# Optimization experiments

Measured on AMD Instinct MI355X. Metric: run time of the kernel, lower is better.

The kernel has to match this reference:

```python
import jax, jax.numpy as jnp
import numpy as np

LN_EPS = 1e-3  # keras LayerNormalization default epsilon
LEAKY_SLOPE = 0.2  # tf 'leaky_relu' default alpha


def layer_norm(x, gamma, beta):
    mu = jnp.mean(x, axis=-1, keepdims=True)
    var = jnp.mean(jnp.square(x - mu), axis=-1, keepdims=True)
    return (x - mu) * jax.lax.rsqrt(var + LN_EPS) * gamma + beta


def attention_head(q_in, kv_in, Wk, Wv, Wq, causal):
    # q_in: [b, sq, d], kv_in: [b, sk, d]
    K = jnp.einsum('bsd,de->bse', kv_in, Wk)
    V = jnp.einsum('bsd,de->bse', kv_in, Wv)
    Q = jnp.einsum('bsd,de->bse', q_in, Wq)
    sk = K.shape[1]
    # NOTE: original scales by sqrt(window_size_keys), i.e. key seq length
    scores = jnp.einsum('bqe,bke->bqk', Q, K) / jnp.sqrt(jnp.float32(sk))
    if causal:
        sq = Q.shape[1]
        mask = jnp.triu(jnp.full((sq, sk), -jnp.inf, dtype=scores.dtype), k=1)
        scores = scores + mask
    probs = jax.nn.softmax(scores, axis=-1)
    return jnp.einsum('bqk,bke->bqe', probs, V)


def setup_inputs() -> dict:
    key = jax.random.key(0)
    ks = jax.random.split(key, 12)
    B, S, D, H = 4, 4096, 256, 400
    p = lambda k, shp: jax.random.normal(k, shp, dtype=jnp.float32) * 0.1
    return {
        'inputs': jax.random.normal(ks[0], (B, S, D), dtype=jnp.float32),
        'context_sequence': jax.random.normal(ks[1], (B, S, D), dtype=jnp.float32),
        'sa_Wk': p(ks[2], (D, D)),
        'sa_Wv': p(ks[3], (D, D)),
        'sa_Wq': p(ks[4], (D, D)),
        'ca_Wk': p(ks[5], (D, D)),
        'ca_Wv': p(ks[6], (D, D)),
        'ca_Wq': p(ks[7], (D, D)),
        'W1': p(ks[8], (D, H)),
        'b1': jnp.zeros((H,), dtype=jnp.float32),
        'W2': p(ks[9], (H, D)),
        'b2': jnp.zeros((D,), dtype=jnp.float32),
        'gamma': jnp.ones((D,), dtype=jnp.float32),
        'beta': jnp.zeros((D,), dtype=jnp.float32),
    }


def reference(inputs, context_sequence, sa_Wk, sa_Wv, sa_Wq, ca_Wk, ca_Wv, ca_Wq,
              W1, b1, W2, b2, gamma, beta):
    # 1) masked self-attention + residual + LN (shared LN params)
    in_attn = attention_head(inputs, inputs, sa_Wk, sa_Wv, sa_Wq, causal=True)
    x = layer_norm(in_attn + inputs, gamma, beta)
    # 2) unmasked cross-attention (queries = x, keys/values = context) + residual + LN
    ctx_attn = attention_head(x, context_sequence, ca_Wk, ca_Wv, ca_Wq, causal=False)
    y = layer_norm(ctx_attn + x, gamma, beta)
    # 3) FFN (Dense 400 leaky_relu -> Dense emb) + residual + LN
    h = jax.nn.leaky_relu(jnp.einsum('bsd,dh->bsh', y, W1) + b1, negative_slope=LEAKY_SLOPE)
    ff = jnp.einsum('bsh,hd->bsd', h, W2) + b2
    return layer_norm(ff + y, gamma, beta)
```

## Files before the change

kernel.cpp:

```cpp
#include <hip/hip_runtime.h>

typedef __bf16  bf16x4 __attribute__((ext_vector_type(4)));
typedef __bf16  bf16x8 __attribute__((ext_vector_type(8)));
typedef float   f32x4  __attribute__((ext_vector_type(4)));
typedef unsigned int u32;

constexpr int BM = 128, BN = 128, BK = 32;

__device__ __forceinline__ void async_cp16(const __bf16* g, __bf16* lds) {
    __builtin_amdgcn_global_load_lds(
        (const __attribute__((address_space(1))) u32*)g,
        (__attribute__((address_space(3))) u32*)lds, 16, 0, 0);
}

__device__ __forceinline__ int swz(int row, int q) {
    return row * BK + (((q + (row >> 1)) & 3) << 3);
}

template<int EPI>
__launch_bounds__(256)
__global__ void gemm_nt(const __bf16* __restrict__ Aall, const __bf16* __restrict__ Ball,
                        const float* __restrict__ bias,
                        void* __restrict__ C0, void* __restrict__ C1, void* __restrict__ C2,
                        int N, int K, long ldb, long sA, long sB, long sC,
                        int nTx, int klen, long pstrideB)
{
    const int bx = blockIdx.x;
    const int chunk = bx / nTx;
    const int n0 = (bx - chunk * nTx) * BN;
    const int m0 = blockIdx.y * BM;
    const int bz = blockIdx.z;
    const int kbase = chunk * klen;

    const __bf16* A  = Aall + (long)bz * sA;
    const __bf16* Bt = Ball + (long)bz * sB;

    __shared__ alignas(16) __bf16 As[BM * BK];
    __shared__ alignas(16) __bf16 Bs[BN * BK];

    const int tid = threadIdx.x;
    const int wave = tid >> 6, lane = tid & 63;
    const int wm = (wave >> 1) * 64, wn = (wave & 1) * 64;
    const int quad = lane >> 4, l16 = lane & 15;

    const int row0 = tid >> 2, sl0 = tid & 3;
    const int ks0 = (sl0 - (row0 >> 1)) & 3;
    const int row1 = row0 + 64;
    const int ks1 = (sl0 - (row1 >> 1)) & 3;
    const __bf16* gA0 = A  + (long)(m0 + row0) * K + kbase + ks0 * 8;
    const __bf16* gA1 = A  + (long)(m0 + row1) * K + kbase + ks1 * 8;
    const __bf16* gB0 = Bt + (long)(n0 + row0) * ldb + kbase + ks0 * 8;
    const __bf16* gB1 = Bt + (long)(n0 + row1) * ldb + kbase + ks1 * 8;
    __bf16* ldsA0 = As + wave * 512;
    __bf16* ldsA1 = As + 2048 + wave * 512;
    __bf16* ldsB0 = Bs + wave * 512;
    __bf16* ldsB1 = Bs + 2048 + wave * 512;

    f32x4 acc[4][4];
    #pragma unroll
    for (int i = 0; i < 4; i++)
        #pragma unroll
        for (int j = 0; j < 4; j++) { f32x4 z = {0.f, 0.f, 0.f, 0.f}; acc[i][j] = z; }

    for (int kk = 0; kk < klen; kk += BK) {
        __syncthreads();
        async_cp16(gA0, ldsA0);
        async_cp16(gA1, ldsA1);
        async_cp16(gB0, ldsB0);
        async_cp16(gB1, ldsB1);
        gA0 += BK; gA1 += BK; gB0 += BK; gB1 += BK;
        __syncthreads();

        bf16x8 af[4], bg[4];
        #pragma unroll
        for (int i = 0; i < 4; i++) {
            af[i] = *(const bf16x8*)(As + swz(wm + i * 16 + l16, quad));
            bg[i] = *(const bf16x8*)(Bs + swz(wn + i * 16 + l16, quad));
        }
        #pragma unroll
        for (int i = 0; i < 4; i++)
            #pragma unroll
            for (int j = 0; j < 4; j++)
                acc[i][j] = __builtin_amdgcn_mfma_f32_16x16x32_bf16(af[i], bg[j], acc[i][j], 0, 0, 0);
    }

    char* cb = (char*)C0 + (EPI == 3 ? (long)chunk * pstrideB : 0);
    #pragma unroll
    for (int j = 0; j < 4; j++) {
        const int col = n0 + wn + j * 16 + l16;
        const float bv = (EPI == 2) ? bias[col] : 0.f;
        #pragma unroll
        for (int i = 0; i < 4; i++) {
            #pragma unroll
            for (int r = 0; r < 4; r++) {
                const int row = m0 + wm + i * 16 + quad * 4 + r;
                float c = acc[i][j][r];
                if (EPI == 2) { c += bv; c = c > 0.f ? c : 0.2f * c; }
                if (EPI == 1 || EPI == 3)
                    ((__bf16*)cb)[(long)bz * sC + (long)row * N + col] = (__bf16)c;
                else if (EPI == 2)
                    ((__bf16*)cb)[(long)row * N + col] = (__bf16)c;
                else {
                    const int seg = col >> 8;
                    __bf16* dst = seg == 0 ? (__bf16*)C0 : (seg == 1 ? (__bf16*)C1 : (__bf16*)C2);
                    dst[(long)row * 256 + (col & 255)] = (__bf16)c;
                }
            }
        }
    }
}

template<int CAUSAL>
__launch_bounds__(512, 4)
__global__ void fattn(const __bf16* __restrict__ Qall, const __bf16* __restrict__ Kall,
                      const __bf16* __restrict__ Vt,
                      __bf16* __restrict__ pbuf, float* __restrict__ side,
                      int NS, long pstrideE, float scale)
{
    constexpr int S = 4096, D = 256, R = 16384;
    const int mt = CAUSAL ? (int)(gridDim.x - 1 - blockIdx.x) : (int)blockIdx.x;
    const int chunk = blockIdx.y;
    const int bz = blockIdx.z;
    const int m0 = mt * 64;

    const int T = CAUSAL ? ((m0 + 64) >> 5) : (S >> 5);
    const int t0 = chunk * T / NS;
    const int t1 = (chunk + 1) * T / NS;
    const int kbase = t0 << 5;
    const int ntile = t1 - t0;

    const __bf16* Q  = Qall + ((long)bz * S + m0) * D;
    const __bf16* Kp = Kall + (long)bz * S * D;
    const long vcol0 = (long)bz * S;

    __shared__ alignas(16) __bf16 Ks[2][8192];
    __shared__ alignas(16) __bf16 Vs[2][8192];
    __shared__ alignas(16) __bf16 Ps[64 * 32];
    __shared__ float sred[8][16];

    const int tid = threadIdx.x;
    const int wave = tid >> 6, lane = tid & 63;
    const int quad = lane >> 4, l16 = lane & 15;
    const int wq16 = (wave >> 1) * 16;
    const int wk16 = (wave & 1) * 16;
    const int we = (wave & 1) * 128;

    bf16x8 qf[8];
    #pragma unroll
    for (int kd = 0; kd < 8; kd++)
        qf[kd] = *(const bf16x8*)(Q + (long)(wq16 + l16) * D + kd * 32 + quad * 8);

    const int srowK = (tid >> 2) & 31;
    const int srowV = tid >> 2;
    const int ks8 = (((tid & 3) - (tid >> 3)) & 3) << 3;
    const int wbase = (tid & ~63) * 8;

    f32x4 acc[8];
    #pragma unroll
    for (int j = 0; j < 8; j++) { f32x4 z = {0.f, 0.f, 0.f, 0.f}; acc[j] = z; }
    float se[4] = {0.f, 0.f, 0.f, 0.f};

    auto stage = [&](int buf, int kb) {
        const __bf16* gK = Kp + (long)(kb + srowK) * D + ks8 + ((tid >> 7) << 5);
        async_cp16(gK,       Ks[buf] + wbase);
        async_cp16(gK + 128, Ks[buf] + 4096 + wbase);
        const __bf16* gV = Vt + vcol0 + kb + ks8 + (long)srowV * R;
        async_cp16(gV,                 Vs[buf] + wbase);
        async_cp16(gV + (long)128 * R, Vs[buf] + 4096 + wbase);
    };

    if (ntile > 0) stage(0, kbase);

    for (int t = 0; t < ntile; ++t) {
        const int cur = t & 1;
        const int kb = kbase + (t << 5);
        __syncthreads();
        if (t + 1 < ntile) stage(cur ^ 1, kb + 32);

        const __bf16* Kb_ = Ks[cur];
        const __bf16* Vb_ = Vs[cur];

        f32x4 sacc = {0.f, 0.f, 0.f, 0.f};
        #pragma unroll
        for (int kd = 0; kd < 8; kd++) {
            bf16x8 b0 = *(const bf16x8*)(Kb_ + kd * 1024 + swz(wk16 + l16, quad));
            sacc = __builtin_amdgcn_mfma_f32_16x16x32_bf16(qf[kd], b0, sacc, 0, 0, 0);
        }

        const bool diag = CAUSAL && (kb >= m0);
        const int kloc = wk16 + l16;
        #pragma unroll
        for (int r = 0; r < 4; r++) {
            const int qloc = wq16 + quad * 4 + r;
            float e = __expf(sacc[r] * scale);
            if (diag && kb + kloc > m0 + qloc) e = 0.f;
            se[r] += e;
            Ps[qloc * 32 + (((kloc >> 3) ^ ((qloc >> 1) & 3)) << 3) + (kloc & 7)] = (__bf16)e;
        }
        __syncthreads();

        {
            const int q0 = wq16 + l16;
            bf16x8 pa = *(const bf16x8*)(Ps + q0 * 32 + ((quad ^ ((q0 >> 1) & 3)) << 3));
            #pragma unroll
            for (int jn = 0; jn < 8; jn++) {
                bf16x8 vb = *(const bf16x8*)(Vb_ + swz(we + jn * 16 + l16, quad));
                acc[jn] = __builtin_amdgcn_mfma_f32_16x16x32_bf16(pa, vb, acc[jn], 0, 0, 0);
            }
        }
    }

    #pragma unroll
    for (int st = 1; st < 16; st <<= 1)
        #pragma unroll
        for (int r = 0; r < 4; r++) se[r] += __shfl_xor(se[r], st);
    if (l16 == 0)
        #pragma unroll
        for (int r = 0; r < 4; r++)
            sred[wave][quad * 4 + r] = se[r];
    __syncthreads();
    if ((wave & 1) == 0 && l16 == 0) {
        float* sd = side + ((long)bz * 64 + chunk) * 4096 + m0 + wq16;
        #pragma unroll
        for (int r = 0; r < 4; r++) {
            const int idx = quad * 4 + r;
            sd[idx] = sred[wave][idx] + sred[wave + 1][idx];
        }
    }

    __bf16* cb = pbuf + (long)chunk * pstrideE + ((long)bz * S + m0) * D;
    #pragma unroll
    for (int jn = 0; jn < 8; jn++) {
        const int col = we + jn * 16 + l16;
        #pragma unroll
        for (int r = 0; r < 4; r++)
            cb[(long)(wq16 + quad * 4 + r) * D + col] = (__bf16)acc[jn][r];
    }
}

template<int NP>
__launch_bounds__(256)
__global__ void ln_res(const __bf16* __restrict__ p, long pstr,
                       const float* __restrict__ resid,
                       const float* __restrict__ side, int lim,
                       const float* __restrict__ bias,
                       const float* __restrict__ gamma, const float* __restrict__ beta,
                       float* __restrict__ outf, __bf16* __restrict__ outb)
{
    const int row  = blockIdx.x * 4 + (threadIdx.x >> 6);
    const int lane = threadIdx.x & 63;
    const long vi = (long)row * 64 + lane;
    float p0 = 0.f, p1 = 0.f, p2 = 0.f, p3 = 0.f;
    #pragma unroll
    for (int i = 0; i < NP; i++) {
        bf16x4 vp = ((const bf16x4*)(p + (long)i * pstr))[vi];
        p0 += (float)vp[0]; p1 += (float)vp[1]; p2 += (float)vp[2]; p3 += (float)vp[3];
    }
    if (side) {
        const float* sp = side + (long)(row >> 12) * 64 * 4096 + (row & 4095);
        float sv = 0.f;
        for (int t = 0; t < lim; t++) sv += sp[(long)t * 4096];
        const float iv = 1.f / sv;
        p0 *= iv; p1 *= iv; p2 *= iv; p3 *= iv;
    }
    float4 vr = ((const float4*)resid)[vi];
    float x0 = vr.x + p0, x1 = vr.y + p1, x2 = vr.z + p2, x3 = vr.w + p3;
    if (bias) {
        float4 vb = ((const float4*)bias)[lane];
        x0 += vb.x; x1 += vb.y; x2 += vb.z; x3 += vb.w;
    }
    float s = x0 + x1 + x2 + x3;
    #pragma unroll
    for (int off = 32; off; off >>= 1) s += __shfl_xor(s, off);
    const float mu = s * (1.f / 256.f);
    float d0 = x0 - mu, d1 = x1 - mu, d2 = x2 - mu, d3 = x3 - mu;
    float s2 = d0 * d0 + d1 * d1 + d2 * d2 + d3 * d3;
    #pragma unroll
    for (int off = 32; off; off >>= 1) s2 += __shfl_xor(s2, off);
    const float rs = rsqrtf(s2 * (1.f / 256.f) + 1e-3f);
    const float4 g  = ((const float4*)gamma)[lane];
    const float4 be = ((const float4*)beta)[lane];
    float o0 = d0 * rs * g.x + be.x, o1 = d1 * rs * g.y + be.y;
    float o2 = d2 * rs * g.z + be.z, o3 = d3 * rs * g.w + be.w;
    float4 o; o.x = o0; o.y = o1; o.z = o2; o.w = o3;
    ((float4*)outf)[vi] = o;
    if (outb) {
        bf16x4 ob; ob[0] = (__bf16)o0; ob[1] = (__bf16)o1; ob[2] = (__bf16)o2; ob[3] = (__bf16)o3;
        ((bf16x4*)outb)[vi] = ob;
    }
}

__device__ __forceinline__ void tp(const float* __restrict__ src, __bf16* __restrict__ dst,
                                   int rows, int cols, int rowsP, int i)
{
    const int c = i / rowsP, r = i - c * rowsP;
    const float v = (r < rows && c < cols) ? src[r * cols + c] : 0.f;
    dst[i] = (__bf16)v;
}

__global__ void prep_all(const float4* __restrict__ inA, const float4* __restrict__ inC,
                         bf16x4* __restrict__ outA, bf16x4* __restrict__ outC,
                         const float* __restrict__ sWq, const float* __restrict__ sWk,
                         const float* __restrict__ sWv,
                         const float* __restrict__ cWq, const float* __restrict__ cWk,
                         const float* __restrict__ cWv,
                         const float* __restrict__ W1, const float* __restrict__ W2,
                         __bf16* __restrict__ wqk_s, __bf16* __restrict__ wv_s,
                         __bf16* __restrict__ wq_c, __bf16* __restrict__ wk_c,
                         __bf16* __restrict__ wv_c,
                         __bf16* __restrict__ W1t, __bf16* __restrict__ W2t,
                         const float* __restrict__ b1, float* __restrict__ b1p)
{
    const int bx = blockIdx.x, tid = threadIdx.x;
    if (bx < 8192) {
        const bool a = bx < 4096;
        const long j = (long)(a ? bx : bx - 4096) * 256 + tid;
        float4 v = (a ? inA : inC)[j];
        bf16x4 o; o[0] = (__bf16)v.x; o[1] = (__bf16)v.y; o[2] = (__bf16)v.z; o[3] = (__bf16)v.w;
        (a ? outA : outC)[j] = o;
    }
    else if (bx < 8448)  tp(sWq, wqk_s,          256, 256, 256, (bx - 8192)  * 256 + tid);
    else if (bx < 8704)  tp(sWk, wqk_s + 65536,  256, 256, 256, (bx - 8448)  * 256 + tid);
    else if (bx < 8960)  tp(sWv, wv_s,           256, 256, 256, (bx - 8704)  * 256 + tid);
    else if (bx < 9216)  tp(cWq, wq_c,           256, 256, 256, (bx - 8960)  * 256 + tid);
    else if (bx < 9472)  tp(cWk, wk_c,           256, 256, 256, (bx - 9216)  * 256 + tid);
    else if (bx < 9728)  tp(cWv, wv_c,           256, 256, 256, (bx - 9472)  * 256 + tid);
    else if (bx < 10240) tp(W1,  W1t,            256, 400, 256, (bx - 9728)  * 256 + tid);
    else if (bx < 10752) tp(W2,  W2t,            400, 256, 512, (bx - 10240) * 256 + tid);
    else { const int i = (bx - 10752) * 256 + tid; if (i < 512) b1p[i] = (i < 400) ? b1[i] : 0.f; }
}

extern "C" void kernel_launch(void* const* d_in, const int* in_sizes, int n_in,
                              void* d_out, int out_size, void* d_ws, size_t ws_size,
                              hipStream_t stream)
{
    constexpr int B = 4, S = 4096, D = 256, H = 400, Hp = 512;
    constexpr int R = B * S;
    constexpr float SCALE = 1.f / 64.f;
    constexpr int NSc = 2;
    constexpr int NSx = 2;
    constexpr int NSf = 2;

    const float* inputs = (const float*)d_in[0];
    const float* ctx    = (const float*)d_in[1];
    const float* sa_Wk  = (const float*)d_in[2];
    const float* sa_Wv  = (const float*)d_in[3];
    const float* sa_Wq  = (const float*)d_in[4];
    const float* ca_Wk  = (const float*)d_in[5];
    const float* ca_Wv  = (const float*)d_in[6];
    const float* ca_Wq  = (const float*)d_in[7];
    const float* W1     = (const float*)d_in[8];
    const float* b1     = (const float*)d_in[9];
    const float* W2     = (const float*)d_in[10];
    const float* b2     = (const float*)d_in[11];
    const float* gamma  = (const float*)d_in[12];
    const float* beta   = (const float*)d_in[13];
    float* out = (float*)d_out;

    char* ws = (char*)d_ws;
    size_t off = 0;
    auto alloc = [&](size_t bytes) -> char* {
        char* p = ws + off; off += (bytes + 255) & ~size_t(255); return p;
    };
    __bf16* bfA  = (__bf16*)alloc((size_t)R * D * 2);
    __bf16* bfC  = (__bf16*)alloc((size_t)R * D * 2);
    __bf16* Qb   = (__bf16*)alloc((size_t)R * D * 2);
    __bf16* Kb   = (__bf16*)alloc((size_t)R * D * 2);
    __bf16* Vt   = (__bf16*)alloc((size_t)2 * D * R * 2);
    __bf16* h    = (__bf16*)alloc((size_t)R * Hp * 2);
    float*  x    = (float*)alloc((size_t)R * D * 4);
    float*  y    = (float*)alloc((size_t)R * D * 4);
    float*  side = (float*)alloc((size_t)B * 64 * S * 4);
    __bf16* wqk_s = (__bf16*)alloc((size_t)2 * D * D * 2);
    __bf16* wv_s  = (__bf16*)alloc((size_t)D * D * 2);
    __bf16* wv_c  = (__bf16*)alloc((size_t)D * D * 2);
    __bf16* wq_c  = (__bf16*)alloc((size_t)D * D * 2);
    __bf16* wk_c  = (__bf16*)alloc((size_t)D * D * 2);
    __bf16* W1t  = (__bf16*)alloc((size_t)Hp * D * 2);
    __bf16* W2t  = (__bf16*)alloc((size_t)D * Hp * 2);
    float*  b1p  = (float*)alloc((size_t)Hp * 4);

    const size_t PBb = (size_t)R * D * 2;
    __bf16* pbuf = (__bf16*)alloc((size_t)4 * PBb);
    if (off > ws_size) return;
    const long PBe = (long)R * D;

    __bf16* xbf = bfA;
    __bf16* ybf = bfC;

    const dim3 blk(256);
    const dim3 blk512(512);

    auto launch_ln = [&](int np, const float* res, const float* sd, int lim,
                         const float* bias, float* of, __bf16* ob) {
        if (np == 4)      ln_res<4><<<R / 4, blk, 0, stream>>>(pbuf, PBe, res, sd, lim, bias, gamma, beta, of, ob);
        else if (np == 2) ln_res<2><<<R / 4, blk, 0, stream>>>(pbuf, PBe, res, sd, lim, bias, gamma, beta, of, ob);
        else              ln_res<1><<<R / 4, blk, 0, stream>>>(pbuf, PBe, res, sd, lim, bias, gamma, beta, of, ob);
    };

    prep_all<<<10754, blk, 0, stream>>>((const float4*)inputs, (const float4*)ctx,
        (bf16x4*)bfA, (bf16x4*)bfC, sa_Wq, sa_Wk, sa_Wv, ca_Wq, ca_Wk, ca_Wv, W1, W2,
        wqk_s, wv_s, wq_c, wk_c, wv_c, W1t, W2t, b1, b1p);

    gemm_nt<4><<<dim3(4, 128, 1), blk, 0, stream>>>(bfA, wqk_s, nullptr,
        Qb, Kb, nullptr, 2 * D, D, D, 0, 0, 0, 4, D, 0);
    gemm_nt<1><<<dim3(128, 2, 2), blk, 0, stream>>>(wv_s, bfA, nullptr,
        Vt, nullptr, nullptr, R, D, D, (long)D * D, (long)R * D, (long)D * R, 128, D, 0);

    fattn<1><<<dim3(64, NSc, B), blk512, 0, stream>>>(Qb, Kb, Vt, pbuf, side, NSc, PBe, SCALE);
    launch_ln(NSc, inputs, side, NSc, nullptr, x, xbf);

    gemm_nt<1><<<dim3(2, 128, 2), blk, 0, stream>>>(xbf, wq_c, nullptr,
        Qb, nullptr, nullptr, D, D, D, (long)R * D, (long)D * D, (long)R * D, 2, D, 0);

    fattn<0><<<dim3(64, NSx, B), blk512, 0, stream>>>(Qb, Kb, Vt + (size_t)D * R,
        pbuf, side, NSx, PBe, SCALE);
    launch_ln(NSx, x, side, NSx, nullptr, y, ybf);

    gemm_nt<2><<<dim3(4, 128, 1), blk, 0, stream>>>(ybf, W1t, b1p,
        h, nullptr, nullptr, Hp, D, D, 0, 0, 0, 4, D, 0);
    gemm_nt<3><<<dim3(2 * NSf, 128, 1), blk, 0, stream>>>(h, W2t, nullptr,
        pbuf, nullptr, nullptr, D, Hp, Hp, 0, 0, 0, 2, Hp / NSf, (long)PBb);
    launch_ln(NSf, y, nullptr, 0, b2, out, nullptr);
}
```

Before: 398.2 us.

## Enlarge attention query tile to 128 rows with per-wave private P tiles

The attention kernel now gives each of its 8 waves 16 query rows across all 32 keys and all 256 output columns, so a block covers 128 queries instead of 64. Each loaded K/V tile is reused by twice as many queries, halving K/V global traffic. Because each wave owns a private slice of the P buffer, the mid-tile block barrier and the cross-wave row-sum reduction go away. The cost is double the accumulator registers (16 f32x4 per thread) under a 512x4 launch bound, which may spill or lower occupancy. The key split count rises from 2 to 4 to keep the grid size up, which adds more partial outputs for the layer-norm pass to combine.

```diff
diff --git a/kernel.cpp b/kernel.cpp
--- a/kernel.cpp
+++ b/kernel.cpp
@@ -121,9 +121,9 @@
     const int mt = CAUSAL ? (int)(gridDim.x - 1 - blockIdx.x) : (int)blockIdx.x;
     const int chunk = blockIdx.y;
     const int bz = blockIdx.z;
-    const int m0 = mt * 64;
-
-    const int T = CAUSAL ? ((m0 + 64) >> 5) : (S >> 5);
+    const int m0 = mt * 128;
+
+    const int T = CAUSAL ? ((m0 + 128) >> 5) : (S >> 5);
     const int t0 = chunk * T / NS;
     const int t1 = (chunk + 1) * T / NS;
     const int kbase = t0 << 5;
@@ -135,15 +135,12 @@
 
     __shared__ alignas(16) __bf16 Ks[2][8192];
     __shared__ alignas(16) __bf16 Vs[2][8192];
-    __shared__ alignas(16) __bf16 Ps[64 * 32];
-    __shared__ float sred[8][16];
+    __shared__ alignas(16) __bf16 Ps[8][512];
 
     const int tid = threadIdx.x;
     const int wave = tid >> 6, lane = tid & 63;
     const int quad = lane >> 4, l16 = lane & 15;
-    const int wq16 = (wave >> 1) * 16;
-    const int wk16 = (wave & 1) * 16;
-    const int we = (wave & 1) * 128;
+    const int wq16 = wave * 16;
 
     bf16x8 qf[8];
     #pragma unroll
@@ -155,9 +152,9 @@
     const int ks8 = (((tid & 3) - (tid >> 3)) & 3) << 3;
     const int wbase = (tid & ~63) * 8;
 
-    f32x4 acc[8];
-    #pragma unroll
-    for (int j = 0; j < 8; j++) { f32x4 z = {0.f, 0.f, 0.f, 0.f}; acc[j] = z; }
+    f32x4 acc[16];
+    #pragma unroll
+    for (int j = 0; j < 16; j++) { f32x4 z = {0.f, 0.f, 0.f, 0.f}; acc[j] = z; }
     float se[4] = {0.f, 0.f, 0.f, 0.f};
 
     auto stage = [&](int buf, int kb) {
@@ -180,62 +177,54 @@
         const __bf16* Kb_ = Ks[cur];
         const __bf16* Vb_ = Vs[cur];
 
-        f32x4 sacc = {0.f, 0.f, 0.f, 0.f};
+        f32x4 s0 = {0.f, 0.f, 0.f, 0.f}, s1 = {0.f, 0.f, 0.f, 0.f};
         #pragma unroll
         for (int kd = 0; kd < 8; kd++) {
-            bf16x8 b0 = *(const bf16x8*)(Kb_ + kd * 1024 + swz(wk16 + l16, quad));
-            sacc = __builtin_amdgcn_mfma_f32_16x16x32_bf16(qf[kd], b0, sacc, 0, 0, 0);
+            bf16x8 k0 = *(const bf16x8*)(Kb_ + kd * 1024 + swz(l16, quad));
+            bf16x8 k1 = *(const bf16x8*)(Kb_ + kd * 1024 + swz(16 + l16, quad));
+            s0 = __builtin_amdgcn_mfma_f32_16x16x32_bf16(qf[kd], k0, s0, 0, 0, 0);
+            s1 = __builtin_amdgcn_mfma_f32_16x16x32_bf16(qf[kd], k1, s1, 0, 0, 0);
         }
 
-        const bool diag = CAUSAL && (kb >= m0);
-        const int kloc = wk16 + l16;
-        #pragma unroll
-        for (int r = 0; r < 4; r++) {
-            const int qloc = wq16 + quad * 4 + r;
-            float e = __expf(sacc[r] * scale);
-            if (diag && kb + kloc > m0 + qloc) e = 0.f;
-            se[r] += e;
-            Ps[qloc * 32 + (((kloc >> 3) ^ ((qloc >> 1) & 3)) << 3) + (kloc & 7)] = (__bf16)e;
-        }
-        __syncthreads();
-
-        {
-            const int q0 = wq16 + l16;
-            bf16x8 pa = *(const bf16x8*)(Ps + q0 * 32 + ((quad ^ ((q0 >> 1) & 3)) << 3));
+        const bool diag = CAUSAL && (kb + 31 > m0 + wq16);
+        __bf16* Pw = Ps[wave];
+        #pragma unroll
+        for (int j = 0; j < 2; j++) {
             #pragma unroll
-            for (int jn = 0; jn < 8; jn++) {
-                bf16x8 vb = *(const bf16x8*)(Vb_ + swz(we + jn * 16 + l16, quad));
-                acc[jn] = __builtin_amdgcn_mfma_f32_16x16x32_bf16(pa, vb, acc[jn], 0, 0, 0);
+            for (int r = 0; r < 4; r++) {
+                const int kl = j * 16 + l16;
+                const int qr = quad * 4 + r;
+                float e = __expf((j ? s1[r] : s0[r]) * scale);
+                if (diag && kb + kl > m0 + wq16 + qr) e = 0.f;
+                se[r] += e;
+                Pw[qr * 32 + (((kl >> 3) ^ (qr & 3)) << 3) + (kl & 7)] = (__bf16)e;
             }
         }
+
+        bf16x8 pa = *(const bf16x8*)(Pw + l16 * 32 + ((quad ^ (l16 & 3)) << 3));
+        #pragma unroll
+        for (int jn = 0; jn < 16; jn++) {
+            bf16x8 vf = *(const bf16x8*)(Vb_ + swz(jn * 16 + l16, quad));
+            acc[jn] = __builtin_amdgcn_mfma_f32_16x16x32_bf16(pa, vf, acc[jn], 0, 0, 0);
+        }
     }
 
     #pragma unroll
     for (int st = 1; st < 16; st <<= 1)
         #pragma unroll
         for (int r = 0; r < 4; r++) se[r] += __shfl_xor(se[r], st);
-    if (l16 == 0)
+    if (l16 == 0) {
+        float* sd = side + ((long)bz * 64 + chunk) * 4096 + m0 + wq16;
+        #pragma unroll
+        for (int r = 0; r < 4; r++) sd[quad * 4 + r] = se[r];
+    }
+
+    __bf16* cb = pbuf + (long)chunk * pstrideE + ((long)bz * S + m0) * D;
+    #pragma unroll
+    for (int jn = 0; jn < 16; jn++)
         #pragma unroll
         for (int r = 0; r < 4; r++)
-            sred[wave][quad * 4 + r] = se[r];
-    __syncthreads();
-    if ((wave & 1) == 0 && l16 == 0) {
-        float* sd = side + ((long)bz * 64 + chunk) * 4096 + m0 + wq16;
-        #pragma unroll
-        for (int r = 0; r < 4; r++) {
-            const int idx = quad * 4 + r;
-            sd[idx] = sred[wave][idx] + sred[wave + 1][idx];
-        }
-    }
-
-    __bf16* cb = pbuf + (long)chunk * pstrideE + ((long)bz * S + m0) * D;
-    #pragma unroll
-    for (int jn = 0; jn < 8; jn++) {
-        const int col = we + jn * 16 + l16;
-        #pragma unroll
-        for (int r = 0; r < 4; r++)
-            cb[(long)(wq16 + quad * 4 + r) * D + col] = (__bf16)acc[jn][r];
-    }
+            cb[(long)(wq16 + quad * 4 + r) * D + jn * 16 + l16] = (__bf16)acc[jn][r];
 }
 
 template<int NP>
@@ -337,8 +326,8 @@
     constexpr int B = 4, S = 4096, D = 256, H = 400, Hp = 512;
     constexpr int R = B * S;
     constexpr float SCALE = 1.f / 64.f;
-    constexpr int NSc = 2;
-    constexpr int NSx = 2;
+    constexpr int NSc = 4;
+    constexpr int NSx = 4;
     constexpr int NSf = 2;
 
     const float* inputs = (const float*)d_in[0];
@@ -407,13 +396,13 @@
     gemm_nt<1><<<dim3(128, 2, 2), blk, 0, stream>>>(wv_s, bfA, nullptr,
         Vt, nullptr, nullptr, R, D, D, (long)D * D, (long)R * D, (long)D * R, 128, D, 0);
 
-    fattn<1><<<dim3(64, NSc, B), blk512, 0, stream>>>(Qb, Kb, Vt, pbuf, side, NSc, PBe, SCALE);
+    fattn<1><<<dim3(32, NSc, B), blk512, 0, stream>>>(Qb, Kb, Vt, pbuf, side, NSc, PBe, SCALE);
     launch_ln(NSc, inputs, side, NSc, nullptr, x, xbf);
 
     gemm_nt<1><<<dim3(2, 128, 2), blk, 0, stream>>>(xbf, wq_c, nullptr,
         Qb, nullptr, nullptr, D, D, D, (long)R * D, (long)D * D, (long)R * D, 2, D, 0);
 
-    fattn<0><<<dim3(64, NSx, B), blk512, 0, stream>>>(Qb, Kb, Vt + (size_t)D * R,
+    fattn<0><<<dim3(32, NSx, B), blk512, 0, stream>>>(Qb, Kb, Vt + (size_t)D * R,
         pbuf, side, NSx, PBe, SCALE);
     launch_ln(NSx, x, side, NSx, nullptr, y, ybf);
 
```

New measurement: 432.8 us. +8.7%, slower.

## Double-buffer GEMM LDS staging and retile attention PV across waves

Applied to the files above, without the earlier changes.

The GEMM now keeps two LDS buffers and issues the next K-tile's async global-to-LDS copies before computing on the current one, dropping one barrier per iteration so loads overlap the MFMAs. The attention PV product is retiled so each wave computes a 32-query by 64-column block instead of 16 by 128. Each V fragment then feeds two MFMAs, cutting LDS reads of V. The GEMM's LDS footprint doubles, and the single remaining barrier has to cover both the async copy completion and buffer reuse.

```diff
diff --git a/kernel.cpp b/kernel.cpp
--- a/kernel.cpp
+++ b/kernel.cpp
@@ -35,8 +35,8 @@
     const __bf16* A  = Aall + (long)bz * sA;
     const __bf16* Bt = Ball + (long)bz * sB;
 
-    __shared__ alignas(16) __bf16 As[BM * BK];
-    __shared__ alignas(16) __bf16 Bs[BN * BK];
+    __shared__ alignas(16) __bf16 As[2][BM * BK];
+    __shared__ alignas(16) __bf16 Bs[2][BN * BK];
 
     const int tid = threadIdx.x;
     const int wave = tid >> 6, lane = tid & 63;
@@ -51,10 +51,6 @@
     const __bf16* gA1 = A  + (long)(m0 + row1) * K + kbase + ks1 * 8;
     const __bf16* gB0 = Bt + (long)(n0 + row0) * ldb + kbase + ks0 * 8;
     const __bf16* gB1 = Bt + (long)(n0 + row1) * ldb + kbase + ks1 * 8;
-    __bf16* ldsA0 = As + wave * 512;
-    __bf16* ldsA1 = As + 2048 + wave * 512;
-    __bf16* ldsB0 = Bs + wave * 512;
-    __bf16* ldsB1 = Bs + 2048 + wave * 512;
 
     f32x4 acc[4][4];
     #pragma unroll
@@ -62,26 +58,32 @@
         #pragma unroll
         for (int j = 0; j < 4; j++) { f32x4 z = {0.f, 0.f, 0.f, 0.f}; acc[i][j] = z; }
 
+    auto stageg = [&](int buf) {
+        async_cp16(gA0, As[buf] + wave * 512);
+        async_cp16(gA1, As[buf] + 2048 + wave * 512);
+        async_cp16(gB0, Bs[buf] + wave * 512);
+        async_cp16(gB1, Bs[buf] + 2048 + wave * 512);
+        gA0 += BK; gA1 += BK; gB0 += BK; gB1 += BK;
+    };
+
+    stageg(0);
+    int cur = 0;
     for (int kk = 0; kk < klen; kk += BK) {
         __syncthreads();
-        async_cp16(gA0, ldsA0);
-        async_cp16(gA1, ldsA1);
-        async_cp16(gB0, ldsB0);
-        async_cp16(gB1, ldsB1);
-        gA0 += BK; gA1 += BK; gB0 += BK; gB1 += BK;
-        __syncthreads();
+        if (kk + BK < klen) stageg(cur ^ 1);
 
         bf16x8 af[4], bg[4];
         #pragma unroll
         for (int i = 0; i < 4; i++) {
-            af[i] = *(const bf16x8*)(As + swz(wm + i * 16 + l16, quad));
-            bg[i] = *(const bf16x8*)(Bs + swz(wn + i * 16 + l16, quad));
+            af[i] = *(const bf16x8*)(As[cur] + swz(wm + i * 16 + l16, quad));
+            bg[i] = *(const bf16x8*)(Bs[cur] + swz(wn + i * 16 + l16, quad));
         }
         #pragma unroll
         for (int i = 0; i < 4; i++)
             #pragma unroll
             for (int j = 0; j < 4; j++)
                 acc[i][j] = __builtin_amdgcn_mfma_f32_16x16x32_bf16(af[i], bg[j], acc[i][j], 0, 0, 0);
+        cur ^= 1;
     }
 
     char* cb = (char*)C0 + (EPI == 3 ? (long)chunk * pstrideB : 0);
@@ -143,7 +145,8 @@
     const int quad = lane >> 4, l16 = lane & 15;
     const int wq16 = (wave >> 1) * 16;
     const int wk16 = (wave & 1) * 16;
-    const int we = (wave & 1) * 128;
+    const int qh = wave >> 2;
+    const int eq = wave & 3;
 
     bf16x8 qf[8];
     #pragma unroll
@@ -155,9 +158,11 @@
     const int ks8 = (((tid & 3) - (tid >> 3)) & 3) << 3;
     const int wbase = (tid & ~63) * 8;
 
-    f32x4 acc[8];
-    #pragma unroll
-    for (int j = 0; j < 8; j++) { f32x4 z = {0.f, 0.f, 0.f, 0.f}; acc[j] = z; }
+    f32x4 acc[2][4];
+    #pragma unroll
+    for (int i = 0; i < 2; i++)
+        #pragma unroll
+        for (int j = 0; j < 4; j++) { f32x4 z = {0.f, 0.f, 0.f, 0.f}; acc[i][j] = z; }
     float se[4] = {0.f, 0.f, 0.f, 0.f};
 
     auto stage = [&](int buf, int kb) {
@@ -200,12 +205,16 @@
         __syncthreads();
 
         {
-            const int q0 = wq16 + l16;
-            bf16x8 pa = *(const bf16x8*)(Ps + q0 * 32 + ((quad ^ ((q0 >> 1) & 3)) << 3));
+            const int q0 = qh * 32 + l16;
+            const int q1 = q0 + 16;
+            const int sx = ((quad ^ ((q0 >> 1) & 3)) << 3);
+            bf16x8 pa0 = *(const bf16x8*)(Ps + q0 * 32 + sx);
+            bf16x8 pa1 = *(const bf16x8*)(Ps + q1 * 32 + sx);
             #pragma unroll
-            for (int jn = 0; jn < 8; jn++) {
-                bf16x8 vb = *(const bf16x8*)(Vb_ + swz(we + jn * 16 + l16, quad));
-                acc[jn] = __builtin_amdgcn_mfma_f32_16x16x32_bf16(pa, vb, acc[jn], 0, 0, 0);
+            for (int j = 0; j < 4; j++) {
+                bf16x8 vb = *(const bf16x8*)(Vb_ + swz(eq * 64 + j * 16 + l16, quad));
+                acc[0][j] = __builtin_amdgcn_mfma_f32_16x16x32_bf16(pa0, vb, acc[0][j], 0, 0, 0);
+                acc[1][j] = __builtin_amdgcn_mfma_f32_16x16x32_bf16(pa1, vb, acc[1][j], 0, 0, 0);
             }
         }
     }
@@ -230,11 +239,13 @@
 
     __bf16* cb = pbuf + (long)chunk * pstrideE + ((long)bz * S + m0) * D;
     #pragma unroll
-    for (int jn = 0; jn < 8; jn++) {
-        const int col = we + jn * 16 + l16;
-        #pragma unroll
-        for (int r = 0; r < 4; r++)
-            cb[(long)(wq16 + quad * 4 + r) * D + col] = (__bf16)acc[jn][r];
+    for (int j = 0; j < 4; j++) {
+        const int col = eq * 64 + j * 16 + l16;
+        #pragma unroll
+        for (int i = 0; i < 2; i++)
+            #pragma unroll
+            for (int r = 0; r < 4; r++)
+                cb[(long)(qh * 32 + i * 16 + quad * 4 + r) * D + col] = (__bf16)acc[i][j][r];
     }
 }
 
```

Result: faster. 386.4 us (-3.0%).
